# Optimization experiments

Hardware: AMD Instinct MI355X
Metric: run time of the kernel (lower is better)

## Reference

```python
import jax, jax.numpy as jnp
import numpy as np

ND, NS = 50000, 30000
FD = FS = 256
H = 256
E = 1000000
EL = 200000


def _lin_init(key, fan_in, fan_out):
    # torch Linear default: U(-1/sqrt(fan_in), 1/sqrt(fan_in)) for W and b
    kw, kb = jax.random.split(key)
    bound = 1.0 / np.sqrt(fan_in)
    W = jax.random.uniform(kw, (fan_in, fan_out), jnp.float32, -bound, bound)
    b = jax.random.uniform(kb, (fan_out,), jnp.float32, -bound, bound)
    return W, b


def setup_inputs() -> dict:
    key = jax.random.key(0)
    ks = jax.random.split(key, 16)
    x_drug = jax.random.normal(ks[0], (ND, FD), jnp.float32)
    x_disease = jax.random.normal(ks[1], (NS, FS), jnp.float32)
    edge_src = jax.random.randint(ks[2], (E,), 0, ND, jnp.int64)
    edge_dst = jax.random.randint(ks[3], (E,), 0, NS, jnp.int64)
    label_row = jax.random.randint(ks[4], (EL,), 0, ND, jnp.int64)
    label_col = jax.random.randint(ks[5], (EL,), 0, NS, jnp.int64)
    # SAGEConv params per layer per edge type: lin_l (on aggregated src, with bias),
    # lin_r (on dst root, no bias). Edge types: ds = drug->disease, sd = disease->drug (rev).
    Wl1_ds, bl1_ds = _lin_init(ks[6], FD, H)
    Wr1_ds, _ = _lin_init(ks[7], FS, H)
    Wl1_sd, bl1_sd = _lin_init(ks[8], FS, H)
    Wr1_sd, _ = _lin_init(ks[9], FD, H)
    Wl2_ds, bl2_ds = _lin_init(ks[10], H, H)
    Wr2_ds, _ = _lin_init(ks[11], H, H)
    Wl2_sd, bl2_sd = _lin_init(ks[12], H, H)
    Wr2_sd, _ = _lin_init(ks[13], H, H)
    Wdec1, bdec1 = _lin_init(ks[14], 2 * H, H)
    Wdec2, bdec2 = _lin_init(ks[15], H, 1)
    return dict(x_drug=x_drug, x_disease=x_disease,
                edge_src=edge_src, edge_dst=edge_dst,
                label_row=label_row, label_col=label_col,
                Wl1_ds=Wl1_ds, bl1_ds=bl1_ds, Wr1_ds=Wr1_ds,
                Wl1_sd=Wl1_sd, bl1_sd=bl1_sd, Wr1_sd=Wr1_sd,
                Wl2_ds=Wl2_ds, bl2_ds=bl2_ds, Wr2_ds=Wr2_ds,
                Wl2_sd=Wl2_sd, bl2_sd=bl2_sd, Wr2_sd=Wr2_sd,
                Wdec1=Wdec1, bdec1=bdec1, Wdec2=Wdec2, bdec2=bdec2)


def _mean_agg(x_src, src, dst, n_dst):
    # gather source features per edge, mean-scatter into destinations
    msg = x_src[src]                                         # [E, F]
    s = jax.ops.segment_sum(msg, dst, num_segments=n_dst)    # [n_dst, F]
    cnt = jax.ops.segment_sum(jnp.ones_like(dst, x_src.dtype), dst, num_segments=n_dst)
    return s / jnp.maximum(cnt, 1.0)[:, None]


def _sage_layer(x_drug, x_dis, src, dst,
                Wl_ds, bl_ds, Wr_ds, Wl_sd, bl_sd, Wr_sd):
    z_dis = _mean_agg(x_drug, src, dst, NS) @ Wl_ds + bl_ds + x_dis @ Wr_ds
    z_drug = _mean_agg(x_dis, dst, src, ND) @ Wl_sd + bl_sd + x_drug @ Wr_sd
    return z_drug, z_dis


def reference(x_drug, x_disease, edge_src, edge_dst, label_row, label_col,
              Wl1_ds, bl1_ds, Wr1_ds, Wl1_sd, bl1_sd, Wr1_sd,
              Wl2_ds, bl2_ds, Wr2_ds, Wl2_sd, bl2_sd, Wr2_sd,
              Wdec1, bdec1, Wdec2, bdec2):
    # layer 1 (relu)
    zd, zs = _sage_layer(x_drug, x_disease, edge_src, edge_dst,
                         Wl1_ds, bl1_ds, Wr1_ds, Wl1_sd, bl1_sd, Wr1_sd)
    zd, zs = jax.nn.relu(zd), jax.nn.relu(zs)
    # layer 2 (no relu, last layer)
    zd, zs = _sage_layer(zd, zs, edge_src, edge_dst,
                         Wl2_ds, bl2_ds, Wr2_ds, Wl2_sd, bl2_sd, Wr2_sd)
    # edge decoder
    z = jnp.concatenate([zd[label_row], zs[label_col]], axis=-1)  # [EL, 2H]
    h = jax.nn.relu(z @ Wdec1 + bdec1)
    out = (h @ Wdec2 + bdec2).reshape(-1)
    return out
```

## Files before the change

kernel.cpp:

```cpp
#include <hip/hip_runtime.h>
#include <hip/hip_bf16.h>

#define ND 50000
#define NS 30000
#define NE 1000000
#define EL 200000
#define NTOT (NS + ND)
#define SCAN_BLK ((NTOT + 1023) / 1024)

#define RANK_BLKS ((NE + 255) / 256)
#define CONV_BLKS 20000
#define GRP_BLKS (6 * RANK_BLKS)
#define CONV_REM (CONV_BLKS - 5 * RANK_BLKS)
#define TRW4_BLKS 1024
#define COMP_BLKS 64
#define BIAS_BLKS 2
#define MEGA_BLKS (RANK_BLKS + CONV_BLKS + TRW4_BLKS + COMP_BLKS + BIAS_BLKS)

typedef short short8 __attribute__((ext_vector_type(8)));
typedef float f32x4 __attribute__((ext_vector_type(4)));

__device__ __forceinline__ float b2f(unsigned short u) {
    union { unsigned int i; float f; } c; c.i = ((unsigned int)u) << 16; return c.f;
}
__device__ __forceinline__ unsigned short f2b(float f) {
    __hip_bfloat16 h = __float2bfloat16(f);
    union { __hip_bfloat16 h; unsigned short u; } c; c.h = h; return c.u;
}

__device__ __forceinline__ void gload_lds16(const unsigned short* g, unsigned short* l) {
    __builtin_amdgcn_global_load_lds(
        (const __attribute__((address_space(1))) unsigned int*)g,
        (__attribute__((address_space(3))) unsigned int*)l, 16, 0, 0);
}

struct WAll {
    const float* w1[4];
    const float* w2[4];
    const float* wdec1;
    const float* bl2_ds;
    const float* bl2_sd;
};

__global__ void zero_kernel(int* a, int n) {
    int i = blockIdx.x * blockDim.x + threadIdx.x;
    if (i < n) a[i] = 0;
}

__global__ __launch_bounds__(256) void mega_prep(const int* __restrict__ esrc,
                                                 const int* __restrict__ edst,
                                                 int* cnt_drug, int* cnt_dis,
                                                 unsigned short* __restrict__ rank_sd,
                                                 unsigned short* __restrict__ rank_ds,
                                                 const float* __restrict__ xd,
                                                 const float* __restrict__ xs,
                                                 unsigned short* __restrict__ xd_b,
                                                 unsigned short* __restrict__ xs_b,
                                                 WAll wa,
                                                 unsigned short* __restrict__ Wt,
                                                 float* __restrict__ cbuf) {
    const int b = blockIdx.x, t = threadIdx.x;
    int role, idx;
    if (b < GRP_BLKS) {
        int g = b / 6, r = b - g * 6;
        if (r == 0) { role = 0; idx = g; }
        else        { role = 1; idx = g * 5 + r - 1; }
    } else if (b < GRP_BLKS + CONV_REM) {
        role = 1; idx = 5 * RANK_BLKS + (b - GRP_BLKS);
    } else if (b < GRP_BLKS + CONV_REM + TRW4_BLKS) {
        role = 2; idx = b - GRP_BLKS - CONV_REM;
    } else if (b < GRP_BLKS + CONV_REM + TRW4_BLKS + COMP_BLKS) {
        role = 3; idx = b - GRP_BLKS - CONV_REM - TRW4_BLKS;
    } else {
        role = 4; idx = b - GRP_BLKS - CONV_REM - TRW4_BLKS - COMP_BLKS;
    }

    if (role == 0) {
        int i = idx * 256 + t;
        if (i < NE) {
            int s = esrc[i], d = edst[i];
            rank_ds[i] = (unsigned short)atomicAdd(&cnt_dis[d], 1);
            rank_sd[i] = (unsigned short)atomicAdd(&cnt_drug[s], 1);
        }
    } else if (role == 1) {
        int i = (idx * 256 + t) * 4;
        const int NDE = ND * 256;
        if (i < NDE) {
            float4 v = *reinterpret_cast<const float4*>(xd + i);
            ushort4 o; o.x = f2b(v.x); o.y = f2b(v.y); o.z = f2b(v.z); o.w = f2b(v.w);
            *reinterpret_cast<ushort4*>(xd_b + i) = o;
        } else {
            int j = i - NDE;
            float4 v = *reinterpret_cast<const float4*>(xs + j);
            ushort4 o; o.x = f2b(v.x); o.y = f2b(v.y); o.z = f2b(v.z); o.w = f2b(v.w);
            *reinterpret_cast<ushort4*>(xs_b + j) = o;
        }
    } else if (role == 2) {
        int o = idx * 256 + t;
        int mat = o >> 16, i2 = o & 65535;
        int n = i2 >> 8, k = i2 & 255;
        Wt[o] = f2b(wa.w1[mat][k * 256 + n]);
    } else if (role == 3) {
        int mat = idx >> 4;
        int k0 = (idx & 15) * 16;
        const float* W2 = wa.w2[mat];
        const float* Wd = wa.wdec1 + ((mat < 2) ? 65536 : 0);
        float acc[16] = {};
        const int n = t;
        for (int j = 0; j < 256; ++j) {
            float wd = Wd[j * 256 + n];
#pragma unroll
            for (int k = 0; k < 16; ++k) acc[k] += W2[(k0 + k) * 256 + j] * wd;
        }
        unsigned short* dst = Wt + (size_t)(4 + mat) * 65536 + n * 256 + k0;
#pragma unroll
        for (int k = 0; k < 16; ++k) dst[k] = f2b(acc[k]);
    } else {
        const float* bsrc = idx ? wa.bl2_sd : wa.bl2_ds;
        const float* Wd = wa.wdec1 + (idx ? 0 : 65536);
        float acc = 0.f;
        const int n = t;
        for (int j = 0; j < 256; ++j) acc += bsrc[j] * Wd[j * 256 + n];
        cbuf[idx * 256 + n] = acc;
    }
}


__global__ __launch_bounds__(256) void scan_part(const int* __restrict__ cnt,
                                                 int* __restrict__ bsum) {
    __shared__ int red[4];
    int t = threadIdx.x, lane = t & 63, wid = t >> 6;
    int base = blockIdx.x * 1024 + t * 4;
    int s = 0;
    if (base < NTOT) {
        int4 c = *reinterpret_cast<const int4*>(cnt + base);
        s = c.x + c.y + c.z + c.w;
    }
#pragma unroll
    for (int off = 32; off; off >>= 1) s += __shfl_down(s, off);
    if (lane == 0) red[wid] = s;
    __syncthreads();
    if (t == 0) bsum[blockIdx.x] = red[0] + red[1] + red[2] + red[3];
}

__global__ void scan_top(int* bsum, int nb) {
    int lane = threadIdx.x;
    int a0 = lane < nb ? bsum[lane] : 0;
    int a1 = (64 + lane) < nb ? bsum[64 + lane] : 0;
    int i0 = a0, i1 = a1;
#pragma unroll
    for (int off = 1; off < 64; off <<= 1) {
        int t0 = __shfl_up(i0, off);
        int t1 = __shfl_up(i1, off);
        if (lane >= off) { i0 += t0; i1 += t1; }
    }
    int tot0 = __shfl(i0, 63);
    if (lane < nb) bsum[lane] = i0 - a0;
    if (64 + lane < nb) bsum[64 + lane] = tot0 + i1 - a1;
}

__global__ __launch_bounds__(256) void scan_emit(const int* __restrict__ cnt,
                                                 const int* __restrict__ boff,
                                                 int* __restrict__ row_dis,
                                                 int* __restrict__ row_drug,
                                                 float* __restrict__ inv_dis,
                                                 float* __restrict__ inv_drug) {
    __shared__ int wsum[4];
    int t = threadIdx.x, lane = t & 63, wid = t >> 6;
    int base = blockIdx.x * 1024 + t * 4;
    int4 c = make_int4(0, 0, 0, 0);
    if (base < NTOT) c = *reinterpret_cast<const int4*>(cnt + base);
    int sl = c.x + c.y + c.z + c.w;
    int sc = sl;
#pragma unroll
    for (int off = 1; off < 64; off <<= 1) {
        int tv = __shfl_up(sc, off);
        if (lane >= off) sc += tv;
    }
    if (lane == 63) wsum[wid] = sc;
    __syncthreads();
    int woff = 0;
    for (int w2 = 0; w2 < wid; ++w2) woff += wsum[w2];
    int run = boff[blockIdx.x] + woff + (sc - sl);
    int cc[4] = { c.x, c.y, c.z, c.w };
    if (base < NTOT) {
#pragma unroll
        for (int k = 0; k < 4; ++k) {
            int i = base + k;
            float iv = 1.0f / (float)(cc[k] > 1 ? cc[k] : 1);
            if (i < NS) { row_dis[i] = run; inv_dis[i] = iv; }
            else        { row_drug[i - NS] = run - NE; inv_drug[i - NS] = iv; }
            run += cc[k];
        }
    }
    if (blockIdx.x == 0 && t == 0) { row_dis[NS] = NE; row_drug[ND] = NE; }
}

__global__ void place_kernel(const int* __restrict__ src, const int* __restrict__ dst,
                             const int* __restrict__ row_drug, const int* __restrict__ row_dis,
                             const unsigned short* __restrict__ rank_sd,
                             const unsigned short* __restrict__ rank_ds,
                             unsigned short* __restrict__ val_sd,
                             unsigned short* __restrict__ val_ds, int n) {
    int i = blockIdx.x * blockDim.x + threadIdx.x;
    if (i < n) {
        int s = src[i], d = dst[i];
        val_ds[row_dis[d] + (int)rank_ds[i]] = (unsigned short)s;
        val_sd[row_drug[s] + (int)rank_sd[i]] = (unsigned short)d;
    }
}


__global__ __launch_bounds__(256) void agg_bf2(const unsigned short* __restrict__ srcDis,
                                               const unsigned short* __restrict__ srcDrug,
                                               const int* __restrict__ row_dis,
                                               const int* __restrict__ row_drug,
                                               const unsigned short* __restrict__ val_ds,
                                               const unsigned short* __restrict__ val_sd,
                                               const float* __restrict__ inv_dis,
                                               const float* __restrict__ inv_drug,
                                               unsigned short* __restrict__ outDis,
                                               unsigned short* __restrict__ outDrug) {
    int wid = threadIdx.x >> 6, lane = threadIdx.x & 63;
    int node = blockIdx.x * 4 + wid;
    const int half = lane >> 5;
    const int sub = lane & 31;
    const unsigned short* xsrc; const int* row; const unsigned short* vals;
    const float* inv; unsigned short* outp;
    if (node < NS) {
        xsrc = srcDis; row = row_dis; vals = val_ds; inv = inv_dis; outp = outDis;
    } else {
        node -= NS;
        if (node >= ND) return;
        xsrc = srcDrug; row = row_drug; vals = val_sd; inv = inv_drug; outp = outDrug;
    }
    const int beg = row[node], end = row[node + 1];
    const int off = sub * 8;
    float a[8] = {};
    int j = beg;
    for (; j + 8 <= end; j += 8) {
        int r0 = vals[j     + half];
        int r1 = vals[j + 2 + half];
        int r2 = vals[j + 4 + half];
        int r3 = vals[j + 6 + half];
        short8 v0 = *reinterpret_cast<const short8*>(xsrc + r0 * 256 + off);
        short8 v1 = *reinterpret_cast<const short8*>(xsrc + r1 * 256 + off);
        short8 v2 = *reinterpret_cast<const short8*>(xsrc + r2 * 256 + off);
        short8 v3 = *reinterpret_cast<const short8*>(xsrc + r3 * 256 + off);
#pragma unroll
        for (int k = 0; k < 8; ++k)
            a[k] += b2f((unsigned short)v0[k]) + b2f((unsigned short)v1[k])
                  + b2f((unsigned short)v2[k]) + b2f((unsigned short)v3[k]);
    }
    for (; j + 2 <= end; j += 2) {
        int r = vals[j + half];
        short8 v = *reinterpret_cast<const short8*>(xsrc + r * 256 + off);
#pragma unroll
        for (int k = 0; k < 8; ++k) a[k] += b2f((unsigned short)v[k]);
    }
    if (j < end && half == 0) {
        int r = vals[j];
        short8 v = *reinterpret_cast<const short8*>(xsrc + r * 256 + off);
#pragma unroll
        for (int k = 0; k < 8; ++k) a[k] += b2f((unsigned short)v[k]);
    }
#pragma unroll
    for (int k = 0; k < 8; ++k) a[k] += __shfl_xor(a[k], 32);
    if (half == 0) {
        const float iv = inv[node];
        short8 o;
#pragma unroll
        for (int k = 0; k < 8; ++k) o[k] = (short)f2b(a[k] * iv);
        *reinterpret_cast<short8*>(outp + node * 256 + off) = o;
    }
}


struct GemmSeg {
    const unsigned short* A1;
    const unsigned short* A2;
    const unsigned short* B1t;
    const unsigned short* B2t;
    const float* bias;
    unsigned short* C;
    int M; int relu; int nblk; int nsteps;
};

__global__ __launch_bounds__(256) void gemm_lds(GemmSeg sa, GemmSeg sb) {
    __shared__ unsigned short As[128 * 64];
    __shared__ unsigned short Bs[128 * 64];
    GemmSeg s;
    int bx = blockIdx.x;
    if (bx < sa.nblk) s = sa;
    else { s = sb; bx -= sa.nblk; }

    const int t = threadIdx.x;
    const int lane = t & 63, w = t >> 6;
    const int wr = w >> 1, wc = w & 1;
    const int fr = lane & 15, g = lane >> 4;
    const int bm0 = bx * 128;
    const int n0b = (int)blockIdx.y * 128;
    const int M = s.M;
    const int r8 = lane >> 3, slotL = lane & 7;

    f32x4 acc[4][4];
#pragma unroll
    for (int m = 0; m < 4; ++m)
#pragma unroll
        for (int n = 0; n < 4; ++n)
            acc[m][n] = (f32x4){0.f, 0.f, 0.f, 0.f};

    for (int st = 0; st < s.nsteps; ++st) {
        const int k0 = (st & 3) * 64;
        const unsigned short* Ap = (st & 4) ? s.A2 : s.A1;
        const unsigned short* Bp = (st & 4) ? s.B2t : s.B1t;
#pragma unroll
        for (int j = 0; j < 4; ++j) {
            const int is = w * 4 + j;
            const int row = is * 8 + r8;
            const int sl = slotL ^ (row & 7);
            int ra = bm0 + row; if (ra >= M) ra = M - 1;
            gload_lds16(Ap + (size_t)ra * 256 + k0 + sl * 8, &As[is * 512]);
            gload_lds16(Bp + (size_t)(n0b + row) * 256 + k0 + sl * 8, &Bs[is * 512]);
        }
        __syncthreads();
#pragma unroll
        for (int kc = 0; kc < 2; ++kc) {
            const int q = kc * 4 + g;
            short8 a[4], b[4];
#pragma unroll
            for (int n = 0; n < 4; ++n) {
                const int br = wc * 64 + n * 16 + fr;
                b[n] = *reinterpret_cast<const short8*>(&Bs[br * 64 + (q ^ (fr & 7)) * 8]);
            }
#pragma unroll
            for (int m = 0; m < 4; ++m) {
                const int ar = wr * 64 + m * 16 + fr;
                a[m] = *reinterpret_cast<const short8*>(&As[ar * 64 + (q ^ (fr & 7)) * 8]);
            }
#pragma unroll
            for (int m = 0; m < 4; ++m)
#pragma unroll
                for (int n = 0; n < 4; ++n)
                    acc[m][n] = __builtin_amdgcn_mfma_f32_16x16x32_bf16(a[m], b[n], acc[m][n], 0, 0, 0);
        }
        __syncthreads();
    }

#pragma unroll
    for (int n = 0; n < 4; ++n) {
        const int col = n0b + wc * 64 + n * 16 + fr;
        const float bv = s.bias ? s.bias[col] : 0.0f;
#pragma unroll
        for (int m = 0; m < 4; ++m) {
#pragma unroll
            for (int r = 0; r < 4; ++r) {
                int row = bm0 + wr * 64 + m * 16 + g * 4 + r;
                if (row < M) {
                    float v = acc[m][n][r] + bv;
                    if (s.relu) v = fmaxf(v, 0.f);
                    s.C[row * 256 + col] = f2b(v);
                }
            }
        }
    }
}


__global__ __launch_bounds__(256) void dec_edge(const unsigned short* __restrict__ Pd,
                                                const unsigned short* __restrict__ Ps,
                                                const int* __restrict__ lrow,
                                                const int* __restrict__ lcol,
                                                const float* __restrict__ b1,
                                                const float* __restrict__ w2,
                                                const float* __restrict__ b2,
                                                float* __restrict__ outp, int n) {
    int wid = threadIdx.x >> 6, lane = threadIdx.x & 63;
    int half = lane >> 5, sl = lane & 31;
    int e = blockIdx.x * 8 + wid * 2 + half;
    if (e >= n) return;
    int r = lrow[e], c = lcol[e];
    const int off = sl * 8;
    short8 pd = *reinterpret_cast<const short8*>(Pd + r * 256 + off);
    short8 ps = *reinterpret_cast<const short8*>(Ps + c * 256 + off);
    float s = 0.f;
#pragma unroll
    for (int k = 0; k < 8; ++k) {
        float h = b2f((unsigned short)pd[k]) + b2f((unsigned short)ps[k]) + b1[off + k];
        s += fmaxf(h, 0.f) * w2[off + k];
    }
#pragma unroll
    for (int o = 16; o; o >>= 1) s += __shfl_down(s, o, 32);
    if (sl == 0) outp[e] = s + b2[0];
}


extern "C" void kernel_launch(void* const* d_in, const int* in_sizes, int n_in,
                              void* d_out, int out_size, void* d_ws, size_t ws_size,
                              hipStream_t stream) {
    const float* x_drug = (const float*)d_in[0];
    const float* x_dis  = (const float*)d_in[1];
    const int* esrc = (const int*)d_in[2];
    const int* edst = (const int*)d_in[3];
    const int* lrow = (const int*)d_in[4];
    const int* lcol = (const int*)d_in[5];
    const float* Wl1_ds = (const float*)d_in[6];
    const float* bl1_ds = (const float*)d_in[7];
    const float* Wr1_ds = (const float*)d_in[8];
    const float* Wl1_sd = (const float*)d_in[9];
    const float* bl1_sd = (const float*)d_in[10];
    const float* Wr1_sd = (const float*)d_in[11];
    const float* Wl2_ds = (const float*)d_in[12];
    const float* bl2_ds = (const float*)d_in[13];
    const float* Wr2_ds = (const float*)d_in[14];
    const float* Wl2_sd = (const float*)d_in[15];
    const float* bl2_sd = (const float*)d_in[16];
    const float* Wr2_sd = (const float*)d_in[17];
    const float* Wdec1 = (const float*)d_in[18];
    const float* bdec1 = (const float*)d_in[19];
    const float* Wdec2 = (const float*)d_in[20];
    const float* bdec2 = (const float*)d_in[21];
    float* outp = (float*)d_out;

    char* ws = (char*)d_ws;
    size_t off = 0;
    auto alloc = [&](size_t bytes) -> void* {
        void* p = ws + off;
        off = (off + bytes + 255) & ~(size_t)255;
        return p;
    };
    int* cnt       = (int*)alloc((size_t)NTOT * 4);
    int* bsum      = (int*)alloc((size_t)SCAN_BLK * 4);
    int* row_dis   = (int*)alloc((size_t)(NS + 1) * 4);
    int* row_drug  = (int*)alloc((size_t)(ND + 1) * 4);
    float* inv_dis = (float*)alloc((size_t)NS * 4);
    float* inv_drug= (float*)alloc((size_t)ND * 4);
    float* cbuf    = (float*)alloc((size_t)512 * 4);
    unsigned short* rank_ds = (unsigned short*)alloc((size_t)NE * 2);
    unsigned short* rank_sd = (unsigned short*)alloc((size_t)NE * 2);
    unsigned short* val_ds  = (unsigned short*)alloc((size_t)NE * 2);
    unsigned short* val_sd  = (unsigned short*)alloc((size_t)NE * 2);
    unsigned short* Wt   = (unsigned short*)alloc((size_t)8 * 65536 * 2);
    unsigned short* xd_b = (unsigned short*)alloc((size_t)ND * 256 * 2);
    unsigned short* xs_b = (unsigned short*)alloc((size_t)NS * 256 * 2);
    unsigned short* aggs = (unsigned short*)alloc((size_t)NS * 256 * 2);
    unsigned short* aggd = (unsigned short*)alloc((size_t)ND * 256 * 2);
    unsigned short* zd1  = (unsigned short*)alloc((size_t)ND * 256 * 2);
    unsigned short* zs1  = (unsigned short*)alloc((size_t)NS * 256 * 2);
    unsigned short* Pd   = (unsigned short*)alloc((size_t)ND * 256 * 2);
    unsigned short* Ps   = (unsigned short*)alloc((size_t)NS * 256 * 2);
    int* cnt_dis = cnt;
    int* cnt_drug = cnt + NS;

    zero_kernel<<<(NTOT + 255) / 256, 256, 0, stream>>>(cnt, NTOT);

    WAll wa;
    wa.w1[0] = Wl1_ds; wa.w1[1] = Wr1_ds; wa.w1[2] = Wl1_sd; wa.w1[3] = Wr1_sd;
    wa.w2[0] = Wl2_ds; wa.w2[1] = Wr2_ds; wa.w2[2] = Wl2_sd; wa.w2[3] = Wr2_sd;
    wa.wdec1 = Wdec1; wa.bl2_ds = bl2_ds; wa.bl2_sd = bl2_sd;
    mega_prep<<<MEGA_BLKS, 256, 0, stream>>>(esrc, edst, cnt_drug, cnt_dis,
                                             rank_sd, rank_ds,
                                             x_drug, x_dis, xd_b, xs_b,
                                             wa, Wt, cbuf);
    unsigned short* WT[8];
    for (int i = 0; i < 8; ++i) WT[i] = Wt + (size_t)i * 65536;

    scan_part<<<SCAN_BLK, 256, 0, stream>>>(cnt, bsum);
    scan_top<<<1, 64, 0, stream>>>(bsum, SCAN_BLK);
    scan_emit<<<SCAN_BLK, 256, 0, stream>>>(cnt, bsum, row_dis, row_drug, inv_dis, inv_drug);
    place_kernel<<<(NE + 255) / 256, 256, 0, stream>>>(esrc, edst, row_drug, row_dis,
                                                       rank_sd, rank_ds, val_sd, val_ds, NE);

    const int AGG_GRID = (NTOT + 3) / 4;
    const int NB_NS = (NS + 127) / 128, NB_ND = (ND + 127) / 128;
    dim3 gemm_grid(NB_NS + NB_ND, 2);

    agg_bf2<<<AGG_GRID, 256, 0, stream>>>(xd_b, xs_b, row_dis, row_drug, val_ds, val_sd,
                                          inv_dis, inv_drug, aggs, aggd);
    {
        GemmSeg a = { aggs, xs_b, WT[0], WT[1], bl1_ds, zs1, NS, 1, NB_NS, 8 };
        GemmSeg b = { aggd, xd_b, WT[2], WT[3], bl1_sd, zd1, ND, 1, NB_ND, 8 };
        gemm_lds<<<gemm_grid, 256, 0, stream>>>(a, b);
    }

    agg_bf2<<<AGG_GRID, 256, 0, stream>>>(zd1, zs1, row_dis, row_drug, val_ds, val_sd,
                                          inv_dis, inv_drug, aggs, aggd);
    {
        GemmSeg a = { aggs, zs1, WT[4], WT[5], cbuf,       Ps, NS, 0, NB_NS, 8 };
        GemmSeg b = { aggd, zd1, WT[6], WT[7], cbuf + 256, Pd, ND, 0, NB_ND, 8 };
        gemm_lds<<<gemm_grid, 256, 0, stream>>>(a, b);
    }

    dec_edge<<<(EL + 7) / 8, 256, 0, stream>>>(Pd, Ps, lrow, lcol, bdec1, Wdec2, bdec2, outp, EL);
}
```

Measured before the change: 539.8 us.

## Project node features before aggregation and fuse root term, bias, relu into aggregation

Uses linearity of mean aggregation: node features are multiplied by the weight matrices first, and the aggregation then gathers the projected features and adds the root projection, bias and relu in its epilogue. Layer 1's projection GEMMs read the fp32 inputs directly, converting to bf16 while staging into shared memory. They run in the same kernel as the degree-counting atomics, which removes the separate bf16 conversion pass. Both GEMMs now run K=256 instead of 512 but produce four outputs. The aggregation also reads an extra root-projection tensor per node, and rounding order changes slightly.

```diff
diff --git a/kernel.cpp b/kernel.cpp
--- a/kernel.cpp
+++ b/kernel.cpp
@@ -8,14 +8,18 @@
 #define NTOT (NS + ND)
 #define SCAN_BLK ((NTOT + 1023) / 1024)
 
-#define RANK_BLKS ((NE + 255) / 256)
-#define CONV_BLKS 20000
-#define GRP_BLKS (6 * RANK_BLKS)
-#define CONV_REM (CONV_BLKS - 5 * RANK_BLKS)
+#define ZERO_BLKS ((NTOT + 255) / 256)
 #define TRW4_BLKS 1024
 #define COMP_BLKS 64
 #define BIAS_BLKS 2
-#define MEGA_BLKS (RANK_BLKS + CONV_BLKS + TRW4_BLKS + COMP_BLKS + BIAS_BLKS)
+#define WPREP_BLKS (ZERO_BLKS + TRW4_BLKS + COMP_BLKS + BIAS_BLKS)
+
+#define RANK_BLKS ((NE + 255) / 256)
+#define NB_D (391 * 2)
+#define NB_S (235 * 2)
+#define GEMM1_BLKS (2 * NB_D + 2 * NB_S)
+#define MEGA_GRP 1252
+#define MEGA_BLKS (RANK_BLKS + GEMM1_BLKS)
 
 typedef short short8 __attribute__((ext_vector_type(8)));
 typedef float f32x4 __attribute__((ext_vector_type(4)));
@@ -42,65 +46,21 @@
     const float* bl2_sd;
 };
 
-__global__ void zero_kernel(int* a, int n) {
-    int i = blockIdx.x * blockDim.x + threadIdx.x;
-    if (i < n) a[i] = 0;
-}
-
-__global__ __launch_bounds__(256) void mega_prep(const int* __restrict__ esrc,
-                                                 const int* __restrict__ edst,
-                                                 int* cnt_drug, int* cnt_dis,
-                                                 unsigned short* __restrict__ rank_sd,
-                                                 unsigned short* __restrict__ rank_ds,
-                                                 const float* __restrict__ xd,
-                                                 const float* __restrict__ xs,
-                                                 unsigned short* __restrict__ xd_b,
-                                                 unsigned short* __restrict__ xs_b,
-                                                 WAll wa,
-                                                 unsigned short* __restrict__ Wt,
-                                                 float* __restrict__ cbuf) {
-    const int b = blockIdx.x, t = threadIdx.x;
-    int role, idx;
-    if (b < GRP_BLKS) {
-        int g = b / 6, r = b - g * 6;
-        if (r == 0) { role = 0; idx = g; }
-        else        { role = 1; idx = g * 5 + r - 1; }
-    } else if (b < GRP_BLKS + CONV_REM) {
-        role = 1; idx = 5 * RANK_BLKS + (b - GRP_BLKS);
-    } else if (b < GRP_BLKS + CONV_REM + TRW4_BLKS) {
-        role = 2; idx = b - GRP_BLKS - CONV_REM;
-    } else if (b < GRP_BLKS + CONV_REM + TRW4_BLKS + COMP_BLKS) {
-        role = 3; idx = b - GRP_BLKS - CONV_REM - TRW4_BLKS;
-    } else {
-        role = 4; idx = b - GRP_BLKS - CONV_REM - TRW4_BLKS - COMP_BLKS;
-    }
-
-    if (role == 0) {
-        int i = idx * 256 + t;
-        if (i < NE) {
-            int s = esrc[i], d = edst[i];
-            rank_ds[i] = (unsigned short)atomicAdd(&cnt_dis[d], 1);
-            rank_sd[i] = (unsigned short)atomicAdd(&cnt_drug[s], 1);
-        }
-    } else if (role == 1) {
-        int i = (idx * 256 + t) * 4;
-        const int NDE = ND * 256;
-        if (i < NDE) {
-            float4 v = *reinterpret_cast<const float4*>(xd + i);
-            ushort4 o; o.x = f2b(v.x); o.y = f2b(v.y); o.z = f2b(v.z); o.w = f2b(v.w);
-            *reinterpret_cast<ushort4*>(xd_b + i) = o;
-        } else {
-            int j = i - NDE;
-            float4 v = *reinterpret_cast<const float4*>(xs + j);
-            ushort4 o; o.x = f2b(v.x); o.y = f2b(v.y); o.z = f2b(v.z); o.w = f2b(v.w);
-            *reinterpret_cast<ushort4*>(xs_b + j) = o;
-        }
-    } else if (role == 2) {
-        int o = idx * 256 + t;
+
+__global__ __launch_bounds__(256) void wprep(int* __restrict__ cnt, WAll wa,
+                                             unsigned short* __restrict__ Wt,
+                                             float* __restrict__ cbuf) {
+    int b = blockIdx.x, t = threadIdx.x;
+    if (b < ZERO_BLKS) {
+        int i = b * 256 + t;
+        if (i < NTOT) cnt[i] = 0;
+    } else if (b < ZERO_BLKS + TRW4_BLKS) {
+        int o = (b - ZERO_BLKS) * 256 + t;
         int mat = o >> 16, i2 = o & 65535;
         int n = i2 >> 8, k = i2 & 255;
         Wt[o] = f2b(wa.w1[mat][k * 256 + n]);
-    } else if (role == 3) {
+    } else if (b < ZERO_BLKS + TRW4_BLKS + COMP_BLKS) {
+        int idx = b - ZERO_BLKS - TRW4_BLKS;
         int mat = idx >> 4;
         int k0 = (idx & 15) * 16;
         const float* W2 = wa.w2[mat];
@@ -116,12 +76,134 @@
 #pragma unroll
         for (int k = 0; k < 16; ++k) dst[k] = f2b(acc[k]);
     } else {
+        int idx = b - ZERO_BLKS - TRW4_BLKS - COMP_BLKS;
         const float* bsrc = idx ? wa.bl2_sd : wa.bl2_ds;
         const float* Wd = wa.wdec1 + (idx ? 0 : 65536);
         float acc = 0.f;
         const int n = t;
         for (int j = 0; j < 256; ++j) acc += bsrc[j] * Wd[j * 256 + n];
         cbuf[idx * 256 + n] = acc;
+    }
+}
+
+__global__ __launch_bounds__(256) void mega(const int* __restrict__ esrc,
+                                            const int* __restrict__ edst,
+                                            int* cnt_drug, int* cnt_dis,
+                                            unsigned short* __restrict__ rank_sd,
+                                            unsigned short* __restrict__ rank_ds,
+                                            const float* __restrict__ xd,
+                                            const float* __restrict__ xs,
+                                            const unsigned short* __restrict__ Wt,
+                                            unsigned short* __restrict__ PA0,
+                                            unsigned short* __restrict__ RA3,
+                                            unsigned short* __restrict__ PB2,
+                                            unsigned short* __restrict__ RB1) {
+    __shared__ unsigned short As[128 * 64];
+    __shared__ unsigned short Bs[128 * 64];
+    const int b = blockIdx.x, t = threadIdx.x;
+    int role, idx;
+    if (b < 5 * MEGA_GRP) {
+        int g = b / 5, r = b - g * 5;
+        if (r < 3) { role = 0; idx = g * 3 + r; }
+        else       { role = 1; idx = g * 2 + r - 3; }
+    } else {
+        role = 0; idx = 3 * MEGA_GRP + (b - 5 * MEGA_GRP);
+    }
+
+    if (role == 0) {
+        int i = idx * 256 + t;
+        if (i < NE) {
+            int s = esrc[i], d = edst[i];
+            rank_ds[i] = (unsigned short)atomicAdd(&cnt_dis[d], 1);
+            rank_sd[i] = (unsigned short)atomicAdd(&cnt_drug[s], 1);
+        }
+        return;
+    }
+
+    int gi = idx;
+    const float* Xf; const unsigned short* Bt; unsigned short* C; int M;
+    if (gi < NB_D)            { Xf = xd; Bt = Wt + 0 * 65536; C = PA0; M = ND; }
+    else if (gi < 2 * NB_D)   { gi -= NB_D;            Xf = xd; Bt = Wt + 3 * 65536; C = RA3; M = ND; }
+    else if (gi < 2 * NB_D + NB_S) { gi -= 2 * NB_D;   Xf = xs; Bt = Wt + 2 * 65536; C = PB2; M = NS; }
+    else                      { gi -= 2 * NB_D + NB_S; Xf = xs; Bt = Wt + 1 * 65536; C = RB1; M = NS; }
+    const int bm0 = (gi >> 1) * 128;
+    const int n0b = (gi & 1) * 128;
+
+    const int lane = t & 63, w = t >> 6;
+    const int wr = w >> 1, wc = w & 1;
+    const int fr = lane & 15, g = lane >> 4;
+    const int r8 = lane >> 3, slotL = lane & 7;
+    const int ar_ = t >> 1, ah = t & 1;
+    int ra = bm0 + ar_; if (ra >= M) ra = M - 1;
+    const int arm = ar_ & 7;
+
+    f32x4 acc[4][4];
+#pragma unroll
+    for (int m = 0; m < 4; ++m)
+#pragma unroll
+        for (int n = 0; n < 4; ++n)
+            acc[m][n] = (f32x4){0.f, 0.f, 0.f, 0.f};
+
+    for (int st = 0; st < 4; ++st) {
+        const int k0 = st * 64;
+#pragma unroll
+        for (int j = 0; j < 4; ++j) {
+            const int is = w * 4 + j;
+            const int rowb = is * 8 + r8;
+            const int sl = slotL ^ (rowb & 7);
+            gload_lds16(Bt + (size_t)(n0b + rowb) * 256 + k0 + sl * 8, &Bs[is * 512]);
+        }
+        {
+            const float* arow = Xf + (size_t)ra * 256 + k0 + ah * 32;
+            unsigned short* awr = &As[ar_ * 64];
+#pragma unroll
+            for (int q2 = 0; q2 < 4; ++q2) {
+                const int q = ah * 4 + q2;
+                float4 f0 = *reinterpret_cast<const float4*>(arow + q2 * 8);
+                float4 f1 = *reinterpret_cast<const float4*>(arow + q2 * 8 + 4);
+                short8 v;
+                v[0] = (short)f2b(f0.x); v[1] = (short)f2b(f0.y);
+                v[2] = (short)f2b(f0.z); v[3] = (short)f2b(f0.w);
+                v[4] = (short)f2b(f1.x); v[5] = (short)f2b(f1.y);
+                v[6] = (short)f2b(f1.z); v[7] = (short)f2b(f1.w);
+                *reinterpret_cast<short8*>(awr + (q ^ arm) * 8) = v;
+            }
+        }
+        __syncthreads();
+#pragma unroll
+        for (int kc = 0; kc < 2; ++kc) {
+            const int q = kc * 4 + g;
+            short8 a[4], bb[4];
+#pragma unroll
+            for (int n = 0; n < 4; ++n) {
+                const int br = wc * 64 + n * 16 + fr;
+                bb[n] = *reinterpret_cast<const short8*>(&Bs[br * 64 + (q ^ (fr & 7)) * 8]);
+            }
+#pragma unroll
+            for (int m = 0; m < 4; ++m) {
+                const int arr = wr * 64 + m * 16 + fr;
+                a[m] = *reinterpret_cast<const short8*>(&As[arr * 64 + (q ^ (fr & 7)) * 8]);
+            }
+#pragma unroll
+            for (int m = 0; m < 4; ++m)
+#pragma unroll
+                for (int n = 0; n < 4; ++n)
+                    acc[m][n] = __builtin_amdgcn_mfma_f32_16x16x32_bf16(a[m], bb[n], acc[m][n], 0, 0, 0);
+        }
+        __syncthreads();
+    }
+
+#pragma unroll
+    for (int n = 0; n < 4; ++n) {
+        const int col = n0b + wc * 64 + n * 16 + fr;
+#pragma unroll
+        for (int m = 0; m < 4; ++m) {
+#pragma unroll
+            for (int r = 0; r < 4; ++r) {
+                int row = bm0 + wr * 64 + m * 16 + g * 4 + r;
+                if (row < M) C[row * 256 + col] = f2b(acc[m][n][r]);
+            }
+        }
     }
 }
 
@@ -211,28 +293,35 @@
 }
 
 
-__global__ __launch_bounds__(256) void agg_bf2(const unsigned short* __restrict__ srcDis,
-                                               const unsigned short* __restrict__ srcDrug,
-                                               const int* __restrict__ row_dis,
-                                               const int* __restrict__ row_drug,
-                                               const unsigned short* __restrict__ val_ds,
-                                               const unsigned short* __restrict__ val_sd,
-                                               const float* __restrict__ inv_dis,
-                                               const float* __restrict__ inv_drug,
-                                               unsigned short* __restrict__ outDis,
-                                               unsigned short* __restrict__ outDrug) {
+__global__ __launch_bounds__(256) void agg_fused(const unsigned short* __restrict__ gatherDrug,
+                                                 const unsigned short* __restrict__ gatherDis,
+                                                 const int* __restrict__ row_dis,
+                                                 const int* __restrict__ row_drug,
+                                                 const unsigned short* __restrict__ val_ds,
+                                                 const unsigned short* __restrict__ val_sd,
+                                                 const float* __restrict__ inv_dis,
+                                                 const float* __restrict__ inv_drug,
+                                                 const unsigned short* __restrict__ dirDis,
+                                                 const unsigned short* __restrict__ dirDrug,
+                                                 const float* __restrict__ bDis,
+                                                 const float* __restrict__ bDrug,
+                                                 unsigned short* __restrict__ outDis,
+                                                 unsigned short* __restrict__ outDrug,
+                                                 int do_relu) {
     int wid = threadIdx.x >> 6, lane = threadIdx.x & 63;
     int node = blockIdx.x * 4 + wid;
     const int half = lane >> 5;
     const int sub = lane & 31;
     const unsigned short* xsrc; const int* row; const unsigned short* vals;
-    const float* inv; unsigned short* outp;
+    const float* inv; const unsigned short* dirp; const float* bias; unsigned short* outp;
     if (node < NS) {
-        xsrc = srcDis; row = row_dis; vals = val_ds; inv = inv_dis; outp = outDis;
+        xsrc = gatherDrug; row = row_dis; vals = val_ds; inv = inv_dis;
+        dirp = dirDis; bias = bDis; outp = outDis;
     } else {
         node -= NS;
         if (node >= ND) return;
-        xsrc = srcDrug; row = row_drug; vals = val_sd; inv = inv_drug; outp = outDrug;
+        xsrc = gatherDis; row = row_drug; vals = val_sd; inv = inv_drug;
+        dirp = dirDrug; bias = bDrug; outp = outDrug;
     }
     const int beg = row[node], end = row[node + 1];
     const int off = sub * 8;
@@ -268,31 +357,38 @@
     for (int k = 0; k < 8; ++k) a[k] += __shfl_xor(a[k], 32);
     if (half == 0) {
         const float iv = inv[node];
+        short8 dir = *reinterpret_cast<const short8*>(dirp + node * 256 + off);
+        float4 b0 = *reinterpret_cast<const float4*>(bias + off);
+        float4 b1 = *reinterpret_cast<const float4*>(bias + off + 4);
+        float bb[8] = { b0.x, b0.y, b0.z, b0.w, b1.x, b1.y, b1.z, b1.w };
         short8 o;
 #pragma unroll
-        for (int k = 0; k < 8; ++k) o[k] = (short)f2b(a[k] * iv);
+        for (int k = 0; k < 8; ++k) {
+            float v = a[k] * iv + b2f((unsigned short)dir[k]) + bb[k];
+            if (do_relu) v = fmaxf(v, 0.f);
+            o[k] = (short)f2b(v);
+        }
         *reinterpret_cast<short8*>(outp + node * 256 + off) = o;
     }
 }
 
 
-struct GemmSeg {
-    const unsigned short* A1;
-    const unsigned short* A2;
-    const unsigned short* B1t;
-    const unsigned short* B2t;
-    const float* bias;
+struct Seg1 {
+    const unsigned short* A;
+    const unsigned short* Bt;
     unsigned short* C;
-    int M; int relu; int nblk; int nsteps;
+    int M; int nblk;
 };
 
-__global__ __launch_bounds__(256) void gemm_lds(GemmSeg sa, GemmSeg sb) {
+__global__ __launch_bounds__(256) void gemm_lds4(Seg1 s0, Seg1 s1, Seg1 s2, Seg1 s3) {
     __shared__ unsigned short As[128 * 64];
     __shared__ unsigned short Bs[128 * 64];
-    GemmSeg s;
+    Seg1 s;
     int bx = blockIdx.x;
-    if (bx < sa.nblk) s = sa;
-    else { s = sb; bx -= sa.nblk; }
+    if (bx < s0.nblk) s = s0;
+    else if (bx < s0.nblk + s1.nblk) { s = s1; bx -= s0.nblk; }
+    else if (bx < s0.nblk + s1.nblk + s2.nblk) { s = s2; bx -= s0.nblk + s1.nblk; }
+    else { s = s3; bx -= s0.nblk + s1.nblk + s2.nblk; }
 
     const int t = threadIdx.x;
     const int lane = t & 63, w = t >> 6;
@@ -310,18 +406,16 @@
         for (int n = 0; n < 4; ++n)
             acc[m][n] = (f32x4){0.f, 0.f, 0.f, 0.f};
 
-    for (int st = 0; st < s.nsteps; ++st) {
-        const int k0 = (st & 3) * 64;
-        const unsigned short* Ap = (st & 4) ? s.A2 : s.A1;
-        const unsigned short* Bp = (st & 4) ? s.B2t : s.B1t;
+    for (int st = 0; st < 4; ++st) {
+        const int k0 = st * 64;
 #pragma unroll
         for (int j = 0; j < 4; ++j) {
             const int is = w * 4 + j;
             const int row = is * 8 + r8;
             const int sl = slotL ^ (row & 7);
             int ra = bm0 + row; if (ra >= M) ra = M - 1;
-            gload_lds16(Ap + (size_t)ra * 256 + k0 + sl * 8, &As[is * 512]);
-            gload_lds16(Bp + (size_t)(n0b + row) * 256 + k0 + sl * 8, &Bs[is * 512]);
+            gload_lds16(s.A + (size_t)ra * 256 + k0 + sl * 8, &As[is * 512]);
+            gload_lds16(s.Bt + (size_t)(n0b + row) * 256 + k0 + sl * 8, &Bs[is * 512]);
         }
         __syncthreads();
 #pragma unroll
@@ -350,17 +444,12 @@
 #pragma unroll
     for (int n = 0; n < 4; ++n) {
         const int col = n0b + wc * 64 + n * 16 + fr;
-        const float bv = s.bias ? s.bias[col] : 0.0f;
 #pragma unroll
         for (int m = 0; m < 4; ++m) {
 #pragma unroll
             for (int r = 0; r < 4; ++r) {
                 int row = bm0 + wr * 64 + m * 16 + g * 4 + r;
-                if (row < M) {
-                    float v = acc[m][n][r] + bv;
-                    if (s.relu) v = fmaxf(v, 0.f);
-                    s.C[row * 256 + col] = f2b(v);
-                }
+                if (row < M) s.C[row * 256 + col] = f2b(acc[m][n][r]);
             }
         }
     }
@@ -441,29 +530,25 @@
     unsigned short* val_ds  = (unsigned short*)alloc((size_t)NE * 2);
     unsigned short* val_sd  = (unsigned short*)alloc((size_t)NE * 2);
     unsigned short* Wt   = (unsigned short*)alloc((size_t)8 * 65536 * 2);
-    unsigned short* xd_b = (unsigned short*)alloc((size_t)ND * 256 * 2);
-    unsigned short* xs_b = (unsigned short*)alloc((size_t)NS * 256 * 2);
-    unsigned short* aggs = (unsigned short*)alloc((size_t)NS * 256 * 2);
-    unsigned short* aggd = (unsigned short*)alloc((size_t)ND * 256 * 2);
+    unsigned short* PA0  = (unsigned short*)alloc((size_t)ND * 256 * 2);
+    unsigned short* RA3  = (unsigned short*)alloc((size_t)ND * 256 * 2);
+    unsigned short* PB2  = (unsigned short*)alloc((size_t)NS * 256 * 2);
+    unsigned short* RB1  = (unsigned short*)alloc((size_t)NS * 256 * 2);
+    unsigned short* zs1  = (unsigned short*)alloc((size_t)NS * 256 * 2);
     unsigned short* zd1  = (unsigned short*)alloc((size_t)ND * 256 * 2);
-    unsigned short* zs1  = (unsigned short*)alloc((size_t)NS * 256 * 2);
+    unsigned short* Ps   = (unsigned short*)alloc((size_t)NS * 256 * 2);
     unsigned short* Pd   = (unsigned short*)alloc((size_t)ND * 256 * 2);
-    unsigned short* Ps   = (unsigned short*)alloc((size_t)NS * 256 * 2);
     int* cnt_dis = cnt;
     int* cnt_drug = cnt + NS;
-
-    zero_kernel<<<(NTOT + 255) / 256, 256, 0, stream>>>(cnt, NTOT);
 
     WAll wa;
     wa.w1[0] = Wl1_ds; wa.w1[1] = Wr1_ds; wa.w1[2] = Wl1_sd; wa.w1[3] = Wr1_sd;
     wa.w2[0] = Wl2_ds; wa.w2[1] = Wr2_ds; wa.w2[2] = Wl2_sd; wa.w2[3] = Wr2_sd;
     wa.wdec1 = Wdec1; wa.bl2_ds = bl2_ds; wa.bl2_sd = bl2_sd;
-    mega_prep<<<MEGA_BLKS, 256, 0, stream>>>(esrc, edst, cnt_drug, cnt_dis,
-                                             rank_sd, rank_ds,
-                                             x_drug, x_dis, xd_b, xs_b,
-                                             wa, Wt, cbuf);
-    unsigned short* WT[8];
-    for (int i = 0; i < 8; ++i) WT[i] = Wt + (size_t)i * 65536;
+    wprep<<<WPREP_BLKS, 256, 0, stream>>>(cnt, wa, Wt, cbuf);
+
+    mega<<<MEGA_BLKS, 256, 0, stream>>>(esrc, edst, cnt_drug, cnt_dis, rank_sd, rank_ds,
+                                        x_drug, x_dis, Wt, PA0, RA3, PB2, RB1);
 
     scan_part<<<SCAN_BLK, 256, 0, stream>>>(cnt, bsum);
     scan_top<<<1, 64, 0, stream>>>(bsum, SCAN_BLK);
@@ -472,24 +557,27 @@
                                                        rank_sd, rank_ds, val_sd, val_ds, NE);
 
     const int AGG_GRID = (NTOT + 3) / 4;
-    const int NB_NS = (NS + 127) / 128, NB_ND = (ND + 127) / 128;
-    dim3 gemm_grid(NB_NS + NB_ND, 2);
-
-    agg_bf2<<<AGG_GRID, 256, 0, stream>>>(xd_b, xs_b, row_dis, row_drug, val_ds, val_sd,
-                                          inv_dis, inv_drug, aggs, aggd);
+
+    agg_fused<<<AGG_GRID, 256, 0, stream>>>(PA0, PB2, row_dis, row_drug, val_ds, val_sd,
+                                            inv_dis, inv_drug, RB1, RA3, bl1_ds, bl1_sd,
+                                            zs1, zd1, 1);
+
+    unsigned short* G1 = PA0;
+    unsigned short* G4 = RA3;
+    unsigned short* G2 = PB2;
+    unsigned short* G3 = RB1;
     {
-        GemmSeg a = { aggs, xs_b, WT[0], WT[1], bl1_ds, zs1, NS, 1, NB_NS, 8 };
-        GemmSeg b = { aggd, xd_b, WT[2], WT[3], bl1_sd, zd1, ND, 1, NB_ND, 8 };
-        gemm_lds<<<gemm_grid, 256, 0, stream>>>(a, b);
-    }
-
-    agg_bf2<<<AGG_GRID, 256, 0, stream>>>(zd1, zs1, row_dis, row_drug, val_ds, val_sd,
-                                          inv_dis, inv_drug, aggs, aggd);
-    {
-        GemmSeg a = { aggs, zs1, WT[4], WT[5], cbuf,       Ps, NS, 0, NB_NS, 8 };
-        GemmSeg b = { aggd, zd1, WT[6], WT[7], cbuf + 256, Pd, ND, 0, NB_ND, 8 };
-        gemm_lds<<<gemm_grid, 256, 0, stream>>>(a, b);
-    }
+        Seg1 a = { zd1, Wt + (size_t)4 * 65536, G1, ND, 391 };
+        Seg1 b = { zs1, Wt + (size_t)5 * 65536, G2, NS, 235 };
+        Seg1 c = { zs1, Wt + (size_t)6 * 65536, G3, NS, 235 };
+        Seg1 d = { zd1, Wt + (size_t)7 * 65536, G4, ND, 391 };
+        dim3 grid(391 + 235 + 235 + 391, 2);
+        gemm_lds4<<<grid, 256, 0, stream>>>(a, b, c, d);
+    }
+
+    agg_fused<<<AGG_GRID, 256, 0, stream>>>(G1, G3, row_dis, row_drug, val_ds, val_sd,
+                                            inv_dis, inv_drug, G2, G4, cbuf, cbuf + 256,
+                                            Ps, Pd, 0);
 
     dec_edge<<<(EL + 7) / 8, 256, 0, stream>>>(Pd, Ps, lrow, lcol, bdec1, Wdec2, bdec2, outp, EL);
 }
```

After: 527.8 us, median of 2. 1.02x faster.
